# Kernel optimization log

Hardware: AMD Instinct MI355X
Metric: run time of the kernel (lower is better)

## Reference

```python
import jax, jax.numpy as jnp
import numpy as np

SOS = 1
H = 1024   # hidden_size
V = 32000  # vocab_size
B = 64     # batch
S = 50     # encoder (source) length
T = 25     # decode steps (target length)


def setup_inputs() -> dict:
    key = jax.random.key(0)
    ks = jax.random.split(key, 16)
    s = 1.0 / np.sqrt(H)

    def u(k, shape):
        return jax.random.uniform(k, shape, jnp.float32, -s, s)

    return {
        "encoder_outputs": jax.random.normal(ks[0], (B, S, H), jnp.float32),
        "encoder_hidden": jax.random.normal(ks[1], (1, B, H), jnp.float32),
        "target_tensor": jax.random.randint(ks[2], (B, T), 0, V),
        "emb": jax.random.normal(ks[3], (V, H), jnp.float32),       # nn.Embedding
        "Wa": u(ks[4], (H, H)), "ba": u(ks[5], (H,)),               # attention query proj
        "Ua": u(ks[6], (H, H)), "bu": u(ks[7], (H,)),               # attention key proj
        "Va": u(ks[8], (H, 1)), "bv": u(ks[9], (1,)),               # attention score vector
        "W_ih": u(ks[10], (3 * H, 2 * H)), "b_ih": u(ks[11], (3 * H,)),  # GRU input weights
        "W_hh": u(ks[12], (3 * H, H)), "b_hh": u(ks[13], (3 * H,)),     # GRU hidden weights
        "Wout": u(ks[14], (V, H)), "bout": u(ks[15], (V,)),         # output linear
    }


def reference(encoder_outputs, encoder_hidden, target_tensor, emb,
              Wa, ba, Ua, bu, Va, bv, W_ih, b_ih, W_hh, b_hh, Wout, bout):
    # Bahdanau key projection is independent of the decode step: precompute once.
    keys_proj = encoder_outputs @ Ua.T + bu        # [B, S, H]
    h0 = encoder_hidden[0]                         # [B, H]

    # Teacher forcing: input at step i is SOS then target[:, :-1]. (Dropout in eval mode = identity.)
    sos = jnp.full((B, 1), SOS, dtype=target_tensor.dtype)
    tokens = jnp.concatenate([sos, target_tensor[:, :-1]], axis=1).T  # [T, B]

    def step(h, tok):
        x_emb = emb[tok]                                         # [B, H]
        q = h @ Wa.T + ba                                        # [B, H] (query = hidden)
        scores = jnp.tanh(q[:, None, :] + keys_proj) @ Va        # [B, S, 1]
        w = jax.nn.softmax(scores[..., 0] + bv[0], axis=-1)      # [B, S]
        context = jnp.einsum('bs,bsh->bh', w, encoder_outputs)   # [B, H]
        x = jnp.concatenate([x_emb, context], axis=-1)           # [B, 2H]
        gx = x @ W_ih.T + b_ih                                   # [B, 3H]
        gh = h @ W_hh.T + b_hh                                   # [B, 3H]
        rx, zx, nx = jnp.split(gx, 3, axis=-1)                   # PyTorch gate order r,z,n
        rh, zh, nh = jnp.split(gh, 3, axis=-1)
        r = jax.nn.sigmoid(rx + rh)
        z = jax.nn.sigmoid(zx + zh)
        n = jnp.tanh(nx + r * nh)
        h_new = (1.0 - z) * n + z * h
        logits = h_new @ Wout.T + bout                           # [B, V]
        return h_new, logits

    _, logits = jax.lax.scan(step, h0, tokens)                   # [T, B, V]
    return jnp.transpose(logits, (1, 0, 2))                      # [B, T, V]
```

## Files before the change

kernel.cpp:

```cpp
#include <hip/hip_runtime.h>
#include <hip/hip_bf16.h>

#define BB_ 64
#define SS_ 50
#define TT_ 25
#define HH_ 1024
#define VV_ 32000

typedef __bf16 bf16x8 __attribute__((ext_vector_type(8)));
typedef float f32x4 __attribute__((ext_vector_type(4)));
typedef unsigned long long u64;

__device__ __forceinline__ unsigned short f2b(float f) {
  unsigned u = __float_as_uint(f);
  u = (u + 0x7FFFu + ((u >> 16) & 1u)) >> 16;
  return (unsigned short)u;
}
__device__ __forceinline__ float fast_tanh(float x) {
  float e = __expf(2.f * x);
  return 1.f - 2.f / (e + 1.f);
}
__device__ __forceinline__ float fast_sigmoid(float x) {
  return 1.f / (1.f + __expf(-x));
}
__device__ __forceinline__ void gload16(const void* g, void* l) {
  __builtin_amdgcn_global_load_lds((const __attribute__((address_space(1))) void*)g,
                                   (__attribute__((address_space(3))) void*)l, 16, 0, 0);
}
__device__ __forceinline__ bf16x8 ldb8(const unsigned short* p) {
  return *(const bf16x8*)p;
}

__device__ __forceinline__ float cldf(const float* p) {
  return __hip_atomic_load(p, __ATOMIC_RELAXED, __HIP_MEMORY_SCOPE_AGENT);
}
__device__ __forceinline__ void cstf(float* p, float v) {
  __hip_atomic_store(p, v, __ATOMIC_RELAXED, __HIP_MEMORY_SCOPE_AGENT);
}
__device__ __forceinline__ u64 cld8(const u64* p) {
  return __hip_atomic_load(p, __ATOMIC_RELAXED, __HIP_MEMORY_SCOPE_AGENT);
}
__device__ __forceinline__ void cst4(unsigned* p, unsigned v) {
  __hip_atomic_store(p, v, __ATOMIC_RELAXED, __HIP_MEMORY_SCOPE_AGENT);
}
__device__ __forceinline__ unsigned cadd(unsigned* p) {
  return __hip_atomic_fetch_add(p, 1u, __ATOMIC_RELAXED, __HIP_MEMORY_SCOPE_AGENT);
}
__device__ __forceinline__ unsigned cldu(const unsigned* p) {
  return __hip_atomic_load(p, __ATOMIC_RELAXED, __HIP_MEMORY_SCOPE_AGENT);
}

#define CNT_ROOT 256
#define CNT_EPOCH 288
#define CNT_QBAR 320
#define CNT_MINI 384

__device__ __forceinline__ void gbarG(unsigned* cnt, unsigned n) {
  __syncthreads();
  if (threadIdx.x == 0) {
    unsigned g = blockIdx.x & 7u;
    unsigned old = cadd(cnt + g * 32);
    if (old == n * 32u - 1u) {
      unsigned r = cadd(cnt + CNT_ROOT);
      if (r == n * 8u - 1u) cst4(cnt + CNT_EPOCH, n);
    }
    while (cldu(cnt + CNT_EPOCH) < n) __builtin_amdgcn_s_sleep(2);
  }
  __syncthreads();
}

__global__ __launch_bounds__(256) void cvt_bf16(const float* __restrict__ src,
                                                unsigned short* __restrict__ dst, long n) {
  long i = ((long)blockIdx.x * 256 + threadIdx.x) * 4;
  if (i >= n) return;
  float4 v = *(const float4*)(src + i);
  *(ushort4*)(dst + i) = make_ushort4(f2b(v.x), f2b(v.y), f2b(v.z), f2b(v.w));
}

__global__ __launch_bounds__(256) void embed_gather(const int* __restrict__ tgt,
                                                    const float* __restrict__ emb,
                                                    unsigned short* __restrict__ X) {
  long idx = ((long)blockIdx.x * 256 + threadIdx.x) * 4;
  if (idx >= (long)1600 * HH_) return;
  int col = (int)(idx & (HH_ - 1));
  int r = (int)(idx >> 10);
  int t = r % 25;
  int tok = (t == 0) ? 1 : tgt[r - 1];
  float4 v = *(const float4*)(emb + (long)tok * HH_ + col);
  *(ushort4*)(X + idx) = make_ushort4(f2b(v.x), f2b(v.y), f2b(v.z), f2b(v.w));
}

__global__ __launch_bounds__(256) void init_h(const float* __restrict__ eh,
                                              unsigned short* __restrict__ Hb,
                                              unsigned* __restrict__ cnt) {
  if (blockIdx.x == 0) {
    for (int k = threadIdx.x; k < 4096; k += 256) cnt[k] = 0;
  }
  int i = (blockIdx.x * 256 + threadIdx.x) * 4;
  if (i >= BB_ * HH_) return;
  float4 v = *(const float4*)(eh + i);
  *(ushort4*)(Hb + i) = make_ushort4(f2b(v.x), f2b(v.y), f2b(v.z), f2b(v.w));
}

__global__ __launch_bounds__(256) void gemm128_bt(
    const unsigned short* __restrict__ A, const unsigned short* __restrict__ W,
    const float* __restrict__ bias, float* __restrict__ out, long ldo,
    int Mtiles, int ldw, int Mvalid) {
  __shared__ __align__(16) unsigned short As[128 * 32];
  __shared__ __align__(16) unsigned short Bs[128 * 32];
  int nwg = gridDim.x;
  int orig = blockIdx.x;
  int xcd = orig & 7, lid = orig >> 3;
  int qq = nwg >> 3, rr = nwg & 7;
  int wgid = (xcd < rr ? xcd * (qq + 1) : rr * (qq + 1) + (xcd - rr) * qq) + lid;
  int m0 = (wgid % Mtiles) * 128;
  int n0 = (wgid / Mtiles) * 128;
  int tid = threadIdx.x;
  int w = tid >> 6, l = tid & 63;
  int srow = tid >> 2, scg = tid & 3;
  int mw = (w & 1) * 64, nw = (w >> 1) * 64;

  const unsigned short* Ag0 = A + (long)(m0 + srow) * 1024 + scg * 8;
  const unsigned short* Ag1 = Ag0 + 64 * 1024;
  const unsigned short* Wg0 = W + (long)(n0 + srow) * ldw + scg * 8;
  const unsigned short* Wg1 = Wg0 + (long)64 * ldw;
  unsigned short* lA0 = As + tid * 8;
  unsigned short* lA1 = As + 2048 + tid * 8;
  unsigned short* lB0 = Bs + tid * 8;
  unsigned short* lB1 = Bs + 2048 + tid * 8;

  f32x4 zero = {0.f, 0.f, 0.f, 0.f};
  f32x4 acc[4][4];
#pragma unroll
  for (int i = 0; i < 4; ++i)
#pragma unroll
    for (int j = 0; j < 4; ++j) acc[i][j] = zero;

  for (int k0 = 0; k0 < 1024; k0 += 32) {
    __syncthreads();
    gload16(Ag0 + k0, lA0);
    gload16(Ag1 + k0, lA1);
    gload16(Wg0 + k0, lB0);
    gload16(Wg1 + k0, lB1);
    __syncthreads();
    bf16x8 af[4], bg[4];
#pragma unroll
    for (int mt = 0; mt < 4; ++mt)
      af[mt] = ldb8(As + (mw + mt * 16 + (l & 15)) * 32 + (l >> 4) * 8);
#pragma unroll
    for (int nt = 0; nt < 4; ++nt)
      bg[nt] = ldb8(Bs + (nw + nt * 16 + (l & 15)) * 32 + (l >> 4) * 8);
#pragma unroll
    for (int mt = 0; mt < 4; ++mt)
#pragma unroll
      for (int nt = 0; nt < 4; ++nt)
        acc[mt][nt] = __builtin_amdgcn_mfma_f32_16x16x32_bf16(af[mt], bg[nt], acc[mt][nt], 0, 0, 0);
  }

  int lr = (l >> 4) * 4, lc = l & 15;
#pragma unroll
  for (int nt = 0; nt < 4; ++nt) {
    int col = n0 + nw + nt * 16 + lc;
    float bv = bias[col];
#pragma unroll
    for (int mt = 0; mt < 4; ++mt) {
#pragma unroll
      for (int r = 0; r < 4; ++r) {
        int m = m0 + mw + mt * 16 + lr + r;
        if (m < Mvalid) out[(long)m * ldo + col] = acc[mt][nt][r] + bv;
      }
    }
  }
}

__global__ __launch_bounds__(256) void decode_loop(
    const unsigned short* __restrict__ WaB, const unsigned short* __restrict__ WhhB,
    const unsigned short* __restrict__ WihB, const float* __restrict__ ba,
    const float* __restrict__ bhh, const float* __restrict__ Va,
    const float* __restrict__ KEYS, const float* __restrict__ enc,
    const float* __restrict__ GA, const float* __restrict__ ehid,
    float* __restrict__ Qf, float* __restrict__ GHf, float* __restrict__ SC,
    unsigned short* __restrict__ CTXB, unsigned short* __restrict__ Hb,
    unsigned short* __restrict__ HALLB, unsigned* __restrict__ cnt) {
  __shared__ __align__(16) char AsC[16 * 2048];
  __shared__ float qs[1024];
  __shared__ float vas[1024];
  __shared__ float wgt[64];

  const int tid = threadIdx.x, bid = blockIdx.x;
  const int wv = tid >> 6, l = tid & 63;
  const int lc = l & 15, hi = l >> 4, ko = hi * 8, lr4 = hi * 4;

  const int m1 = (bid & 3) * 16;
  const int nch = (bid >> 2) * 4 + wv;
  const int n1 = nch * 16;
  const unsigned short* B1;
  float* o1; long ldo1; float bv1;
  if (n1 < 1024) {
    B1 = WaB + (long)(n1 + lc) * 1024 + ko;
    o1 = Qf + n1; ldo1 = 1024; bv1 = ba[n1 + lc];
  } else {
    B1 = WhhB + (long)(n1 - 1024 + lc) * 1024 + ko;
    o1 = GHf + (n1 - 1024); ldo1 = 3072; bv1 = bhh[n1 - 1024 + lc];
  }

  const int b2 = bid >> 2;
  const int jq = (bid & 3) * 4 + wv;
  const int c2 = (bid & 3) * 256 + tid;

  const int m3 = (bid & 3) * 16, n3 = (bid >> 2) * 16;
  const unsigned short* Bg0 = WihB + (long)(n3 + lc) * 2048 + 1024 + ko;
  const unsigned short* Bg1 = Bg0 + (long)1024 * 2048;
  const unsigned short* Bg2 = Bg0 + (long)2048 * 2048;
  const int ig = n3 + lc;
  float hreg[4];
  if (tid < 64) {
#pragma unroll
    for (int r = 0; r < 4; ++r) hreg[r] = ehid[(long)(m3 + lr4 + r) * HH_ + ig];
  }

#pragma unroll
  for (int j = 0; j < 4; ++j) vas[tid + j * 256] = Va[tid + j * 256];

  const f32x4 zero = {0.f, 0.f, 0.f, 0.f};
  unsigned gB = 0;

  for (int t = 0; t < TT_; ++t) {
    {
#pragma unroll
      for (int i = 0; i < 16; ++i) {
        u64 v = cld8((const u64*)(Hb + (long)(m1 + i) * HH_) + tid);
        *(u64*)(AsC + ((i * 2048 + tid * 8) ^ ((i & 7) << 4))) = v;
      }
      __syncthreads();
      f32x4 acc = zero;
#pragma unroll 8
      for (int k = 0; k < 1024; k += 32) {
        bf16x8 af = *(const bf16x8*)(AsC + ((lc * 2048 + (k + ko) * 2) ^ ((lc & 7) << 4)));
        acc = __builtin_amdgcn_mfma_f32_16x16x32_bf16(af, ldb8(B1 + k), acc, 0, 0, 0);
      }
#pragma unroll
      for (int r = 0; r < 4; ++r)
        cstf(o1 + (long)(m1 + lr4 + r) * ldo1 + lc, acc[r] + bv1);
    }
    __syncthreads();
    if (tid == 0) {
      if (bid < 64) cadd(cnt + CNT_QBAR);
      while (cldu(cnt + CNT_QBAR) < (unsigned)(t + 1) * 64u) __builtin_amdgcn_s_sleep(2);
    }
    __syncthreads();

    {
#pragma unroll
      for (int j = 0; j < 4; ++j)
        qs[tid + j * 256] = cldf(Qf + (long)b2 * HH_ + tid + j * 256);
      __syncthreads();
      for (int s = jq; s < SS_; s += 16) {
        const float* kr = KEYS + ((long)b2 * SS_ + s) * HH_;
        float p = 0.f;
#pragma unroll
        for (int j = 0; j < 16; ++j) {
          int hh = l + j * 64;
          p += fast_tanh(qs[hh] + cldf(kr + hh)) * vas[hh];
        }
#pragma unroll
        for (int off = 32; off; off >>= 1) p += __shfl_down(p, off);
        if (l == 0) cstf(SC + (long)b2 * 64 + s, p);
      }
    }
    __syncthreads();
    if (tid == 0) {
      unsigned* mc = cnt + CNT_MINI + b2 * 32;
      cadd(mc);
      while (cldu(mc) < (unsigned)(t + 1) * 4u) __builtin_amdgcn_s_sleep(2);
    }
    __syncthreads();

    {
      if (tid < 64) {
        float v = (tid < SS_) ? cldf(SC + (long)b2 * 64 + tid) : -1e30f;
        float m = v;
#pragma unroll
        for (int off = 32; off; off >>= 1) m = fmaxf(m, __shfl_down(m, off));
        m = __shfl(m, 0);
        float e = (tid < SS_) ? __expf(v - m) : 0.f;
        float ssum = e;
#pragma unroll
        for (int off = 32; off; off >>= 1) ssum += __shfl_down(ssum, off);
        ssum = __shfl(ssum, 0);
        if (tid < SS_) wgt[tid] = e / ssum;
      }
      __syncthreads();
      {
        const float* ep = enc + (long)b2 * SS_ * HH_ + c2;
        float a0 = 0.f;
#pragma unroll 10
        for (int s = 0; s < SS_; ++s)
          a0 += wgt[s] * cldf(ep + (long)s * HH_);
        unsigned hb16 = (unsigned)f2b(a0);
        unsigned ob = (unsigned)__shfl_xor((int)hb16, 1);
        if ((tid & 1) == 0)
          cst4((unsigned*)(CTXB + (long)b2 * HH_ + c2), hb16 | (ob << 16));
      }
    }
    gbarG(cnt, ++gB);

    {
#pragma unroll
      for (int i = 0; i < 16; ++i) {
        u64 v = cld8((const u64*)(CTXB + (long)(m3 + i) * HH_) + tid);
        *(u64*)(AsC + ((i * 2048 + tid * 8) ^ ((i & 7) << 4))) = v;
      }
      __syncthreads();
      if (tid < 64) {
        f32x4 ar = zero, az = zero, an_ = zero;
#pragma unroll 8
        for (int k = 0; k < 1024; k += 32) {
          bf16x8 a = *(const bf16x8*)(AsC + ((lc * 2048 + (k + ko) * 2) ^ ((lc & 7) << 4)));
          ar = __builtin_amdgcn_mfma_f32_16x16x32_bf16(a, ldb8(Bg0 + k), ar, 0, 0, 0);
          az = __builtin_amdgcn_mfma_f32_16x16x32_bf16(a, ldb8(Bg1 + k), az, 0, 0, 0);
          an_ = __builtin_amdgcn_mfma_f32_16x16x32_bf16(a, ldb8(Bg2 + k), an_, 0, 0, 0);
        }
#pragma unroll
        for (int r = 0; r < 4; ++r) {
          int bb = m3 + lr4 + r;
          long rowBT = (long)bb * TT_ + t;
          const float* ga = GA + rowBT * 3072;
          const float* gh = GHf + (long)bb * 3072;
          float rr = fast_sigmoid(cldf(ga + ig) + ar[r] + cldf(gh + ig));
          float zz = fast_sigmoid(cldf(ga + 1024 + ig) + az[r] + cldf(gh + 1024 + ig));
          float nn = fast_tanh(cldf(ga + 2048 + ig) + an_[r] + rr * cldf(gh + 2048 + ig));
          float hnew = (1.f - zz) * nn + zz * hreg[r];
          hreg[r] = hnew;
          unsigned hb = (unsigned)f2b(hnew);
          unsigned ob = (unsigned)__shfl_xor((int)hb, 1);
          if ((lc & 1) == 0)
            cst4((unsigned*)(Hb + (long)bb * HH_ + ig), hb | (ob << 16));
          HALLB[rowBT * HH_ + ig] = (unsigned short)hb;
        }
      }
    }
    if (t < TT_ - 1) gbarG(cnt, ++gB);
  }
}

extern "C" void kernel_launch(void* const* d_in, const int* in_sizes, int n_in,
                              void* d_out, int out_size, void* d_ws, size_t ws_size,
                              hipStream_t stream) {
  (void)in_sizes; (void)n_in; (void)out_size; (void)ws_size;
  const float* enc  = (const float*)d_in[0];
  const float* ehid = (const float*)d_in[1];
  const int*   tgt  = (const int*)d_in[2];
  const float* emb  = (const float*)d_in[3];
  const float* Wa   = (const float*)d_in[4];
  const float* ba   = (const float*)d_in[5];
  const float* Ua   = (const float*)d_in[6];
  const float* bu   = (const float*)d_in[7];
  const float* Va   = (const float*)d_in[8];
  const float* Wih  = (const float*)d_in[10];
  const float* bih  = (const float*)d_in[11];
  const float* Whh  = (const float*)d_in[12];
  const float* bhh  = (const float*)d_in[13];
  const float* Wout = (const float*)d_in[14];
  const float* bout = (const float*)d_in[15];
  float* out = (float*)d_out;

  char* p = (char*)d_ws;
  auto alloc = [&](size_t bytes) { char* r = p; p += (bytes + 255) & ~(size_t)255; return r; };
  unsigned short* WOUTB = (unsigned short*)alloc((size_t)VV_ * HH_ * 2);
  unsigned short* WIHB  = (unsigned short*)alloc((size_t)3072 * 2048 * 2);
  unsigned short* WHHB  = (unsigned short*)alloc((size_t)3072 * 1024 * 2);
  unsigned short* WAB   = (unsigned short*)alloc((size_t)1024 * 1024 * 2);
  unsigned short* UAB   = (unsigned short*)alloc((size_t)1024 * 1024 * 2);
  unsigned short* ENCB  = (unsigned short*)alloc((size_t)BB_ * SS_ * HH_ * 2);
  unsigned short* XEMB  = (unsigned short*)alloc((size_t)1664 * HH_ * 2);
  unsigned short* HALLB = (unsigned short*)alloc((size_t)1664 * HH_ * 2);
  float* KEYS = (float*)alloc((size_t)BB_ * SS_ * HH_ * 4);
  float* GA   = (float*)alloc((size_t)1600 * 3072 * 4);
  float* GHf  = (float*)alloc((size_t)BB_ * 3072 * 4);
  float* Qf   = (float*)alloc((size_t)BB_ * HH_ * 4);
  float* SCf  = (float*)alloc((size_t)BB_ * 64 * 4);
  unsigned short* Hb = (unsigned short*)alloc((size_t)BB_ * HH_ * 2);
  unsigned short* CTXB = (unsigned short*)alloc((size_t)BB_ * HH_ * 2);
  unsigned* CNT = (unsigned*)alloc(4096 * 4);

  auto cvt = [&](const float* s, unsigned short* d, long n) {
    cvt_bf16<<<dim3((unsigned)((n / 4 + 255) / 256)), dim3(256), 0, stream>>>(s, d, n);
  };
  cvt(Wout, WOUTB, (long)VV_ * HH_);
  cvt(Wih, WIHB, (long)3072 * 2048);
  cvt(Whh, WHHB, (long)3072 * 1024);
  cvt(Wa, WAB, (long)1024 * 1024);
  cvt(Ua, UAB, (long)1024 * 1024);
  cvt(enc, ENCB, (long)BB_ * SS_ * HH_);
  embed_gather<<<dim3(1600 * HH_ / 4 / 256), dim3(256), 0, stream>>>(tgt, emb, XEMB);
  init_h<<<dim3(BB_ * HH_ / 4 / 256), dim3(256), 0, stream>>>(ehid, Hb, CNT);

  gemm128_bt<<<dim3(25 * 8), dim3(256), 0, stream>>>(ENCB, UAB, bu, KEYS, (long)1024, 25, 1024, 3200);
  gemm128_bt<<<dim3(13 * 24), dim3(256), 0, stream>>>(XEMB, WIHB, bih, GA, (long)3072, 13, 2048, 1600);

  decode_loop<<<dim3(256), dim3(256), 0, stream>>>(
      WAB, WHHB, WIHB, ba, bhh, Va, KEYS, enc, GA, ehid,
      Qf, GHf, SCf, CTXB, Hb, HALLB, CNT);

  gemm128_bt<<<dim3(13 * 250), dim3(256), 0, stream>>>(HALLB, WOUTB, bout, out, (long)VV_, 13, 1024, 1600);
}
```

Measured before the change: 1.740 ms.

## Use per-step rotating buffers, bf16 keys/encoder, and XCD-aware block mapping in decode loop

```diff
diff --git a/kernel.cpp b/kernel.cpp
--- a/kernel.cpp
+++ b/kernel.cpp
@@ -16,6 +16,9 @@
   u = (u + 0x7FFFu + ((u >> 16) & 1u)) >> 16;
   return (unsigned short)u;
 }
+__device__ __forceinline__ float b2f_(unsigned short s) {
+  return __uint_as_float((unsigned)s << 16);
+}
 __device__ __forceinline__ float fast_tanh(float x) {
   float e = __expf(2.f * x);
   return 1.f - 2.f / (e + 1.f);
@@ -31,14 +34,8 @@
   return *(const bf16x8*)p;
 }
 
-__device__ __forceinline__ float cldf(const float* p) {
-  return __hip_atomic_load(p, __ATOMIC_RELAXED, __HIP_MEMORY_SCOPE_AGENT);
-}
 __device__ __forceinline__ void cstf(float* p, float v) {
   __hip_atomic_store(p, v, __ATOMIC_RELAXED, __HIP_MEMORY_SCOPE_AGENT);
-}
-__device__ __forceinline__ u64 cld8(const u64* p) {
-  return __hip_atomic_load(p, __ATOMIC_RELAXED, __HIP_MEMORY_SCOPE_AGENT);
 }
 __device__ __forceinline__ void cst4(unsigned* p, unsigned v) {
   __hip_atomic_store(p, v, __ATOMIC_RELAXED, __HIP_MEMORY_SCOPE_AGENT);
@@ -91,7 +88,7 @@
 }
 
 __global__ __launch_bounds__(256) void init_h(const float* __restrict__ eh,
-                                              unsigned short* __restrict__ Hb,
+                                              unsigned short* __restrict__ HBROT,
                                               unsigned* __restrict__ cnt) {
   if (blockIdx.x == 0) {
     for (int k = threadIdx.x; k < 4096; k += 256) cnt[k] = 0;
@@ -99,7 +96,7 @@
   int i = (blockIdx.x * 256 + threadIdx.x) * 4;
   if (i >= BB_ * HH_) return;
   float4 v = *(const float4*)(eh + i);
-  *(ushort4*)(Hb + i) = make_ushort4(f2b(v.x), f2b(v.y), f2b(v.z), f2b(v.w));
+  *(ushort4*)(HBROT + i) = make_ushort4(f2b(v.x), f2b(v.y), f2b(v.z), f2b(v.w));
 }
 
 __global__ __launch_bounds__(256) void gemm128_bt(
@@ -177,10 +174,10 @@
     const unsigned short* __restrict__ WaB, const unsigned short* __restrict__ WhhB,
     const unsigned short* __restrict__ WihB, const float* __restrict__ ba,
     const float* __restrict__ bhh, const float* __restrict__ Va,
-    const float* __restrict__ KEYS, const float* __restrict__ enc,
+    const unsigned short* __restrict__ KEYSB, const unsigned short* __restrict__ ENCB,
     const float* __restrict__ GA, const float* __restrict__ ehid,
-    float* __restrict__ Qf, float* __restrict__ GHf, float* __restrict__ SC,
-    unsigned short* __restrict__ CTXB, unsigned short* __restrict__ Hb,
+    float* __restrict__ QROT, float* __restrict__ GHROT, float* __restrict__ SCROT,
+    unsigned short* __restrict__ CTXROT, unsigned short* __restrict__ HBROT,
     unsigned short* __restrict__ HALLB, unsigned* __restrict__ cnt) {
   __shared__ __align__(16) char AsC[16 * 2048];
   __shared__ float qs[1024];
@@ -190,25 +187,25 @@
   const int tid = threadIdx.x, bid = blockIdx.x;
   const int wv = tid >> 6, l = tid & 63;
   const int lc = l & 15, hi = l >> 4, ko = hi * 8, lr4 = hi * 4;
-
-  const int m1 = (bid & 3) * 16;
-  const int nch = (bid >> 2) * 4 + wv;
+  const int xcd = bid & 7, lxb = bid >> 3;
+  const int mt_ = lxb & 3, cg = lxb >> 2;
+
+  const int m1 = mt_ * 16;
+  const int nch = xcd * 32 + cg * 4 + wv;
   const int n1 = nch * 16;
-  const unsigned short* B1;
-  float* o1; long ldo1; float bv1;
-  if (n1 < 1024) {
-    B1 = WaB + (long)(n1 + lc) * 1024 + ko;
-    o1 = Qf + n1; ldo1 = 1024; bv1 = ba[n1 + lc];
-  } else {
-    B1 = WhhB + (long)(n1 - 1024 + lc) * 1024 + ko;
-    o1 = GHf + (n1 - 1024); ldo1 = 3072; bv1 = bhh[n1 - 1024 + lc];
-  }
-
-  const int b2 = bid >> 2;
-  const int jq = (bid & 3) * 4 + wv;
-  const int c2 = (bid & 3) * 256 + tid;
-
-  const int m3 = (bid & 3) * 16, n3 = (bid >> 2) * 16;
+  const bool isq = (n1 < 1024);
+  const unsigned short* B1 = isq ? WaB + (long)(n1 + lc) * 1024 + ko
+                                 : WhhB + (long)(n1 - 1024 + lc) * 1024 + ko;
+  float* o1 = isq ? QROT + n1 : GHROT + (n1 - 1024);
+  const long ldo1 = isq ? 1024 : 3072;
+  const long slot1 = isq ? (long)BB_ * 1024 : (long)BB_ * 3072;
+  const float bv1 = isq ? ba[n1 + lc] : bhh[n1 - 1024 + lc];
+
+  const int b2 = xcd * 8 + cg;
+  const int jq = mt_ * 4 + wv;
+  const int c2 = mt_ * 256 + tid;
+
+  const int m3 = mt_ * 16, n3 = (xcd * 8 + cg) * 16;
   const unsigned short* Bg0 = WihB + (long)(n3 + lc) * 2048 + 1024 + ko;
   const unsigned short* Bg1 = Bg0 + (long)1024 * 2048;
   const unsigned short* Bg2 = Bg0 + (long)2048 * 2048;
@@ -227,9 +224,10 @@
 
   for (int t = 0; t < TT_; ++t) {
     {
+      const unsigned short* hbase = HBROT + (long)t * (BB_ * 1024);
 #pragma unroll
       for (int i = 0; i < 16; ++i) {
-        u64 v = cld8((const u64*)(Hb + (long)(m1 + i) * HH_) + tid);
+        u64 v = *((const u64*)(hbase + (long)(m1 + i) * 1024) + tid);
         *(u64*)(AsC + ((i * 2048 + tid * 8) ^ ((i & 7) << 4))) = v;
       }
       __syncthreads();
@@ -241,31 +239,32 @@
       }
 #pragma unroll
       for (int r = 0; r < 4; ++r)
-        cstf(o1 + (long)(m1 + lr4 + r) * ldo1 + lc, acc[r] + bv1);
+        cstf(o1 + (long)t * slot1 + (long)(m1 + lr4 + r) * ldo1 + lc, acc[r] + bv1);
     }
     __syncthreads();
     if (tid == 0) {
-      if (bid < 64) cadd(cnt + CNT_QBAR);
+      if (xcd < 2) cadd(cnt + CNT_QBAR);
       while (cldu(cnt + CNT_QBAR) < (unsigned)(t + 1) * 64u) __builtin_amdgcn_s_sleep(2);
     }
     __syncthreads();
 
     {
+      const float* qsl = QROT + (long)t * (BB_ * 1024) + (long)b2 * 1024;
 #pragma unroll
       for (int j = 0; j < 4; ++j)
-        qs[tid + j * 256] = cldf(Qf + (long)b2 * HH_ + tid + j * 256);
+        qs[tid + j * 256] = qsl[tid + j * 256];
       __syncthreads();
       for (int s = jq; s < SS_; s += 16) {
-        const float* kr = KEYS + ((long)b2 * SS_ + s) * HH_;
+        const unsigned short* kr = KEYSB + ((long)b2 * SS_ + s) * 1024;
         float p = 0.f;
 #pragma unroll
         for (int j = 0; j < 16; ++j) {
           int hh = l + j * 64;
-          p += fast_tanh(qs[hh] + cldf(kr + hh)) * vas[hh];
+          p += fast_tanh(qs[hh] + b2f_(kr[hh])) * vas[hh];
         }
 #pragma unroll
         for (int off = 32; off; off >>= 1) p += __shfl_down(p, off);
-        if (l == 0) cstf(SC + (long)b2 * 64 + s, p);
+        if (l == 0) cstf(SCROT + (long)t * 4096 + b2 * 64 + s, p);
       }
     }
     __syncthreads();
@@ -278,7 +277,7 @@
 
     {
       if (tid < 64) {
-        float v = (tid < SS_) ? cldf(SC + (long)b2 * 64 + tid) : -1e30f;
+        float v = (tid < SS_) ? SCROT[(long)t * 4096 + b2 * 64 + tid] : -1e30f;
         float m = v;
 #pragma unroll
         for (int off = 32; off; off >>= 1) m = fmaxf(m, __shfl_down(m, off));
@@ -292,23 +291,24 @@
       }
       __syncthreads();
       {
-        const float* ep = enc + (long)b2 * SS_ * HH_ + c2;
+        const unsigned short* ep = ENCB + (long)b2 * SS_ * 1024 + c2;
         float a0 = 0.f;
 #pragma unroll 10
         for (int s = 0; s < SS_; ++s)
-          a0 += wgt[s] * cldf(ep + (long)s * HH_);
+          a0 += wgt[s] * b2f_(ep[(long)s * 1024]);
         unsigned hb16 = (unsigned)f2b(a0);
         unsigned ob = (unsigned)__shfl_xor((int)hb16, 1);
         if ((tid & 1) == 0)
-          cst4((unsigned*)(CTXB + (long)b2 * HH_ + c2), hb16 | (ob << 16));
+          cst4((unsigned*)(CTXROT + (long)t * (BB_ * 1024) + (long)b2 * 1024 + c2), hb16 | (ob << 16));
       }
     }
     gbarG(cnt, ++gB);
 
     {
+      const unsigned short* cbase = CTXROT + (long)t * (BB_ * 1024);
 #pragma unroll
       for (int i = 0; i < 16; ++i) {
-        u64 v = cld8((const u64*)(CTXB + (long)(m3 + i) * HH_) + tid);
+        u64 v = *((const u64*)(cbase + (long)(m3 + i) * 1024) + tid);
         *(u64*)(AsC + ((i * 2048 + tid * 8) ^ ((i & 7) << 4))) = v;
       }
       __syncthreads();
@@ -321,21 +321,23 @@
           az = __builtin_amdgcn_mfma_f32_16x16x32_bf16(a, ldb8(Bg1 + k), az, 0, 0, 0);
           an_ = __builtin_amdgcn_mfma_f32_16x16x32_bf16(a, ldb8(Bg2 + k), an_, 0, 0, 0);
         }
+        const float* ghb = GHROT + (long)t * (BB_ * 3072);
+        unsigned short* hnb = HBROT + (long)(t + 1) * (BB_ * 1024);
 #pragma unroll
         for (int r = 0; r < 4; ++r) {
           int bb = m3 + lr4 + r;
           long rowBT = (long)bb * TT_ + t;
           const float* ga = GA + rowBT * 3072;
-          const float* gh = GHf + (long)bb * 3072;
-          float rr = fast_sigmoid(cldf(ga + ig) + ar[r] + cldf(gh + ig));
-          float zz = fast_sigmoid(cldf(ga + 1024 + ig) + az[r] + cldf(gh + 1024 + ig));
-          float nn = fast_tanh(cldf(ga + 2048 + ig) + an_[r] + rr * cldf(gh + 2048 + ig));
+          const float* gh = ghb + (long)bb * 3072;
+          float rr = fast_sigmoid(ga[ig] + ar[r] + gh[ig]);
+          float zz = fast_sigmoid(ga[1024 + ig] + az[r] + gh[1024 + ig]);
+          float nn = fast_tanh(ga[2048 + ig] + an_[r] + rr * gh[2048 + ig]);
           float hnew = (1.f - zz) * nn + zz * hreg[r];
           hreg[r] = hnew;
           unsigned hb = (unsigned)f2b(hnew);
           unsigned ob = (unsigned)__shfl_xor((int)hb, 1);
           if ((lc & 1) == 0)
-            cst4((unsigned*)(Hb + (long)bb * HH_ + ig), hb | (ob << 16));
+            cst4((unsigned*)(hnb + (long)bb * 1024 + ig), hb | (ob << 16));
           HALLB[rowBT * HH_ + ig] = (unsigned short)hb;
         }
       }
@@ -376,12 +378,13 @@
   unsigned short* XEMB  = (unsigned short*)alloc((size_t)1664 * HH_ * 2);
   unsigned short* HALLB = (unsigned short*)alloc((size_t)1664 * HH_ * 2);
   float* KEYS = (float*)alloc((size_t)BB_ * SS_ * HH_ * 4);
+  unsigned short* KEYSB = (unsigned short*)alloc((size_t)BB_ * SS_ * HH_ * 2);
   float* GA   = (float*)alloc((size_t)1600 * 3072 * 4);
-  float* GHf  = (float*)alloc((size_t)BB_ * 3072 * 4);
-  float* Qf   = (float*)alloc((size_t)BB_ * HH_ * 4);
-  float* SCf  = (float*)alloc((size_t)BB_ * 64 * 4);
-  unsigned short* Hb = (unsigned short*)alloc((size_t)BB_ * HH_ * 2);
-  unsigned short* CTXB = (unsigned short*)alloc((size_t)BB_ * HH_ * 2);
+  float* QROT  = (float*)alloc((size_t)TT_ * BB_ * 1024 * 4);
+  float* GHROT = (float*)alloc((size_t)TT_ * BB_ * 3072 * 4);
+  float* SCROT = (float*)alloc((size_t)TT_ * 4096 * 4);
+  unsigned short* CTXROT = (unsigned short*)alloc((size_t)TT_ * BB_ * 1024 * 2);
+  unsigned short* HBROT  = (unsigned short*)alloc((size_t)(TT_ + 1) * BB_ * 1024 * 2);
   unsigned* CNT = (unsigned*)alloc(4096 * 4);
 
   auto cvt = [&](const float* s, unsigned short* d, long n) {
@@ -394,14 +397,15 @@
   cvt(Ua, UAB, (long)1024 * 1024);
   cvt(enc, ENCB, (long)BB_ * SS_ * HH_);
   embed_gather<<<dim3(1600 * HH_ / 4 / 256), dim3(256), 0, stream>>>(tgt, emb, XEMB);
-  init_h<<<dim3(BB_ * HH_ / 4 / 256), dim3(256), 0, stream>>>(ehid, Hb, CNT);
+  init_h<<<dim3(BB_ * HH_ / 4 / 256), dim3(256), 0, stream>>>(ehid, HBROT, CNT);
 
   gemm128_bt<<<dim3(25 * 8), dim3(256), 0, stream>>>(ENCB, UAB, bu, KEYS, (long)1024, 25, 1024, 3200);
+  cvt(KEYS, KEYSB, (long)BB_ * SS_ * HH_);
   gemm128_bt<<<dim3(13 * 24), dim3(256), 0, stream>>>(XEMB, WIHB, bih, GA, (long)3072, 13, 2048, 1600);
 
   decode_loop<<<dim3(256), dim3(256), 0, stream>>>(
-      WAB, WHHB, WIHB, ba, bhh, Va, KEYS, enc, GA, ehid,
-      Qf, GHf, SCf, CTXB, Hb, HALLB, CNT);
+      WAB, WHHB, WIHB, ba, bhh, Va, KEYSB, ENCB, GA, ehid,
+      QROT, GHROT, SCROT, CTXROT, HBROT, HALLB, CNT);
 
   gemm128_bt<<<dim3(13 * 250), dim3(256), 0, stream>>>(HALLB, WOUTB, bout, out, (long)VV_, 13, 1024, 1600);
 }
```

Result: faster. 1.657 ms (-4.8%).
